# Optimization experiments

Hardware: AMD Instinct MI355X
Metric: run time of the kernel (lower is better)

The kernel has to match this reference:

```python
import jax, jax.numpy as jnp
import numpy as np

H = 12          # num heads
D = 768         # embed dim
HD = D // H     # head dim
SCALE = HD ** -0.5
NEG = -(3.0 ** 39)  # matches torch's triu(1) * -3.0**39 mask value


def setup_inputs() -> dict:
    key = jax.random.key(0)
    ks = jax.random.split(key, 9)
    B, S = 4, 1024
    lim = 1.0 / np.sqrt(D)
    def lin(k):
        kw, kb = jax.random.split(k)
        W = jax.random.uniform(kw, (D, D), jnp.float32, -lim, lim)  # [out,in]
        b = jax.random.uniform(kb, (D,), jnp.float32, -lim, lim)
        return W, b
    Wq, bq = lin(ks[0]); Wk, bk = lin(ks[1]); Wv, bv = lin(ks[2]); Wo, bo = lin(ks[3])
    hidden_states = jax.random.normal(ks[4], (B, S, D), jnp.float32)
    return {"hidden_states": hidden_states,
            "Wq": Wq, "bq": bq, "Wk": Wk, "bk": bk,
            "Wv": Wv, "bv": bv, "Wo": Wo, "bo": bo}


def reference(hidden_states, Wq, bq, Wk, bk, Wv, bv, Wo, bo):
    B, S, _ = hidden_states.shape
    split = lambda x: x.reshape(B, S, H, HD).transpose(0, 2, 1, 3)  # [B,H,S,HD]
    q = split(hidden_states @ Wq.T + bq) * SCALE
    k = split(hidden_states @ Wk.T + bk)
    v = split(hidden_states @ Wv.T + bv)
    scores = jnp.einsum('bhqd,bhkd->bhqk', q, k)
    causal_mask = jnp.triu(jnp.full((S, S), NEG, hidden_states.dtype), k=1)
    scores = scores + causal_mask  # broadcast over [B,H]
    probs = jax.nn.softmax(scores, axis=-1)
    out = jnp.einsum('bhqk,bhkd->bhqd', probs, v)
    out = out.transpose(0, 2, 1, 3).reshape(B, S, H * HD)
    return out @ Wo.T + bo
```

## Files before the change

kernel.cpp:

```cpp
#include <hip/hip_runtime.h>

#define NH 12
#define DM 768
#define HD 64
#define BB 4
#define SS 1024
#define MTOT (BB*SS)
#define ATT_SCALE 0.125f
#define NEGMASK (-4.0525551530189755e18f)

typedef __attribute__((ext_vector_type(8))) short short8;
typedef __attribute__((ext_vector_type(4))) float floatx4;
typedef __attribute__((ext_vector_type(4))) unsigned short ushort4v;

__device__ __forceinline__ float bf2f(unsigned short u){
    union { unsigned int i; float f; } x; x.i = ((unsigned int)u) << 16; return x.f;
}
__device__ __forceinline__ unsigned short f2bf(float f){
    union { float f; unsigned int i; } x; x.f = f;
    unsigned int i = x.i;
    return (unsigned short)((i + 0x7FFFu + ((i >> 16) & 1u)) >> 16);
}

#define XQ4 (MTOT*DM/4)
#define WQ4 (DM*DM/4)

__global__ __launch_bounds__(256) void convert_bf16(
    const float* __restrict__ X,
    const float* __restrict__ Wq, const float* __restrict__ Wk,
    const float* __restrict__ Wv, const float* __restrict__ Wo,
    unsigned short* __restrict__ Xb,
    unsigned short* __restrict__ Wqb, unsigned short* __restrict__ Wkb,
    unsigned short* __restrict__ Wvb, unsigned short* __restrict__ Wob)
{
    const int idx = blockIdx.x * 256 + threadIdx.x;
    const float* s; unsigned short* d; int off;
    if (idx < XQ4) { s = X; d = Xb; off = idx; }
    else {
        const int r = idx - XQ4;
        const int wsel = r / WQ4;
        off = r - wsel * WQ4;
        s = (wsel==0)?Wq:(wsel==1)?Wk:(wsel==2)?Wv:Wo;
        d = (wsel==0)?Wqb:(wsel==1)?Wkb:(wsel==2)?Wvb:Wob;
    }
    const float4 v = ((const float4*)s)[off];
    ushort4v o;
    o[0] = f2bf(v.x); o[1] = f2bf(v.y); o[2] = f2bf(v.z); o[3] = f2bf(v.w);
    ((ushort4v*)d)[off] = o;
}

__global__ __launch_bounds__(256) void qkv_mfma(
    const unsigned short* __restrict__ Xb,
    const unsigned short* __restrict__ Wqb,
    const unsigned short* __restrict__ Wkb,
    const unsigned short* __restrict__ Wvb,
    const float* __restrict__ bq, const float* __restrict__ bk,
    const float* __restrict__ bv,
    unsigned short* __restrict__ qout,
    unsigned short* __restrict__ kout,
    unsigned short* __restrict__ vout)
{
    const int which = blockIdx.z;
    const int n0 = blockIdx.x * 128;
    const int m0 = blockIdx.y * 128;
    const unsigned short* W = (which==0) ? Wqb : (which==1) ? Wkb : Wvb;
    const float* bias = (which==0) ? bq : (which==1) ? bk : bv;
    unsigned short* out = (which==0) ? qout : (which==1) ? kout : vout;
    const float scl = (which==0) ? ATT_SCALE : 1.0f;

    __shared__ unsigned short As[128*32];
    __shared__ unsigned short Bs[128*32];

    const int t = threadIdx.x;
    const int w = t >> 6, lane = t & 63;
    const int c = lane & 15, g = lane >> 4;
    const int wr = w >> 1, wc = w & 1;

    floatx4 acc[4][4] = {};

    const int srow = lane >> 2;
    const int ske  = (lane & 3) * 8;

    for (int k0 = 0; k0 < DM; k0 += 32) {
        __syncthreads();
        #pragma unroll
        for (int j = 0; j < 2; ++j) {
            const int row = w*32 + j*16 + srow;
            __builtin_amdgcn_global_load_lds(
                (const __attribute__((address_space(1))) unsigned int*)
                    (Xb + (size_t)(m0 + row) * DM + k0 + ske),
                (__attribute__((address_space(3))) unsigned int*)
                    (As + (w*32 + j*16) * 32),
                16, 0, 0);
            __builtin_amdgcn_global_load_lds(
                (const __attribute__((address_space(1))) unsigned int*)
                    (W + (size_t)(n0 + row) * DM + k0 + ske),
                (__attribute__((address_space(3))) unsigned int*)
                    (Bs + (w*32 + j*16) * 32),
                16, 0, 0);
        }
        __syncthreads();

        short8 af[4], bfr[4];
        #pragma unroll
        for (int mi = 0; mi < 4; ++mi)
            af[mi] = *(const short8*)(As + (wr*64 + mi*16 + c)*32 + g*8);
        #pragma unroll
        for (int ni = 0; ni < 4; ++ni)
            bfr[ni] = *(const short8*)(Bs + (wc*64 + ni*16 + c)*32 + g*8);
        #pragma unroll
        for (int mi = 0; mi < 4; ++mi)
            #pragma unroll
            for (int ni = 0; ni < 4; ++ni)
                acc[mi][ni] = __builtin_amdgcn_mfma_f32_16x16x32_bf16(
                    af[mi], bfr[ni], acc[mi][ni], 0, 0, 0);
    }

    #pragma unroll
    for (int mi = 0; mi < 4; ++mi) {
        #pragma unroll
        for (int r = 0; r < 4; ++r) {
            const int m = m0 + wr*64 + mi*16 + g*4 + r;
            const int b = m >> 10, s = m & 1023;
            #pragma unroll
            for (int ni = 0; ni < 4; ++ni) {
                const int n = n0 + wc*64 + ni*16 + c;
                const int h = n >> 6, hd = n & 63;
                const float val = (acc[mi][ni][r] + bias[n]) * scl;
                out[(((size_t)(b*NH + h))*SS + s)*HD + hd] = f2bf(val);
            }
        }
    }
}

__global__ __launch_bounds__(256) void attn_mfma(
    const unsigned short* __restrict__ Q,
    const unsigned short* __restrict__ K,
    const unsigned short* __restrict__ V,
    unsigned short* __restrict__ O)
{
    const int bh = blockIdx.x;
    const int qb = blockIdx.y * 64;
    const unsigned short* Qp = Q + (size_t)bh * SS * HD;
    const unsigned short* Kp = K + (size_t)bh * SS * HD;
    const unsigned short* Vp = V + (size_t)bh * SS * HD;

    __shared__ unsigned short Vt[64 * 72];
    __shared__ unsigned short Pl[4][16 * 72];

    const int t    = threadIdx.x;
    const int w    = t >> 6;
    const int lane = t & 63;
    const int c    = lane & 15;
    const int g    = lane >> 4;

    short8 qf[2];
    #pragma unroll
    for (int st = 0; st < 2; ++st)
        qf[st] = *(const short8*)(Qp + (size_t)(qb + w*16 + c) * HD + g*8 + 32*st);

    floatx4 Oacc[4] = {};
    float m_r[4], l_r[4];
    #pragma unroll
    for (int r = 0; r < 4; ++r) { m_r[r] = -INFINITY; l_r[r] = 0.0f; }

    const int ntile = qb / 64 + 1;
    for (int kt = 0; kt < ntile; ++kt) {
        const int k0 = kt * 64;

        __syncthreads();
        {
            const int kk = t >> 2;
            const int d0 = (t & 3) * 16;
            const unsigned short* vp = Vp + (size_t)(k0 + kk) * HD + d0;
            short8 v0 = *(const short8*)(vp);
            short8 v1 = *(const short8*)(vp + 8);
            #pragma unroll
            for (int j = 0; j < 8; ++j) {
                Vt[(d0 + j    ) * 72 + kk] = (unsigned short)v0[j];
                Vt[(d0 + j + 8) * 72 + kk] = (unsigned short)v1[j];
            }
        }
        __syncthreads();

        floatx4 Sacc[4] = {};
        #pragma unroll
        for (int nf = 0; nf < 4; ++nf) {
            #pragma unroll
            for (int st = 0; st < 2; ++st) {
                const short8 kf = *(const short8*)(Kp + (size_t)(k0 + nf*16 + c) * HD + g*8 + 32*st);
                Sacc[nf] = __builtin_amdgcn_mfma_f32_16x16x32_bf16(qf[st], kf, Sacc[nf], 0, 0, 0);
            }
        }

        if (k0 + 63 > qb + w*16) {
            #pragma unroll
            for (int nf = 0; nf < 4; ++nf) {
                const int col = k0 + nf*16 + c;
                #pragma unroll
                for (int r = 0; r < 4; ++r) {
                    const int row = qb + w*16 + g*4 + r;
                    if (col > row) Sacc[nf][r] += NEGMASK;
                }
            }
        }

        float alpha[4];
        #pragma unroll
        for (int r = 0; r < 4; ++r) {
            float mx = Sacc[0][r];
            mx = fmaxf(mx, Sacc[1][r]);
            mx = fmaxf(mx, Sacc[2][r]);
            mx = fmaxf(mx, Sacc[3][r]);
            #pragma unroll
            for (int msk = 1; msk < 16; msk <<= 1)
                mx = fmaxf(mx, __shfl_xor(mx, msk, 64));
            const float mnew = fmaxf(m_r[r], mx);
            alpha[r] = __expf(m_r[r] - mnew);
            float sum = 0.0f;
            #pragma unroll
            for (int nf = 0; nf < 4; ++nf) {
                const float p = __expf(Sacc[nf][r] - mnew);
                Sacc[nf][r] = p;
                sum += p;
            }
            #pragma unroll
            for (int msk = 1; msk < 16; msk <<= 1)
                sum += __shfl_xor(sum, msk, 64);
            l_r[r] = l_r[r] * alpha[r] + sum;
            m_r[r] = mnew;
            #pragma unroll
            for (int nf = 0; nf < 4; ++nf) Oacc[nf][r] *= alpha[r];
        }

        unsigned short* pw = Pl[w];
        #pragma unroll
        for (int r = 0; r < 4; ++r)
            #pragma unroll
            for (int nf = 0; nf < 4; ++nf)
                pw[(g*4 + r) * 72 + nf*16 + c] = f2bf(Sacc[nf][r]);

        #pragma unroll
        for (int st = 0; st < 2; ++st) {
            const short8 pf = *(const short8*)(pw + c * 72 + g*8 + 32*st);
            #pragma unroll
            for (int nf = 0; nf < 4; ++nf) {
                const short8 vf = *(const short8*)(Vt + (nf*16 + c) * 72 + g*8 + 32*st);
                Oacc[nf] = __builtin_amdgcn_mfma_f32_16x16x32_bf16(pf, vf, Oacc[nf], 0, 0, 0);
            }
        }
    }

    const int b = bh / NH, h = bh % NH;
    #pragma unroll
    for (int r = 0; r < 4; ++r) {
        const float inv = 1.0f / l_r[r];
        const int s = qb + w*16 + g*4 + r;
        #pragma unroll
        for (int nf = 0; nf < 4; ++nf)
            O[((size_t)(b*SS + s))*DM + h*HD + nf*16 + c] = f2bf(Oacc[nf][r] * inv);
    }
}

__global__ __launch_bounds__(256) void out_mfma(
    const unsigned short* __restrict__ A,
    const unsigned short* __restrict__ Wb,
    const float* __restrict__ bias,
    float* __restrict__ outf)
{
    const int n0 = blockIdx.x * 128;
    const int m0 = blockIdx.y * 128;

    __shared__ unsigned short As[128*32];
    __shared__ unsigned short Bs[128*32];

    const int t = threadIdx.x;
    const int w = t >> 6, lane = t & 63;
    const int c = lane & 15, g = lane >> 4;
    const int wr = w >> 1, wc = w & 1;

    floatx4 acc[4][4] = {};

    const int srow = lane >> 2;
    const int ske  = (lane & 3) * 8;

    for (int k0 = 0; k0 < DM; k0 += 32) {
        __syncthreads();
        #pragma unroll
        for (int j = 0; j < 2; ++j) {
            const int row = w*32 + j*16 + srow;
            __builtin_amdgcn_global_load_lds(
                (const __attribute__((address_space(1))) unsigned int*)
                    (A + (size_t)(m0 + row) * DM + k0 + ske),
                (__attribute__((address_space(3))) unsigned int*)
                    (As + (w*32 + j*16) * 32),
                16, 0, 0);
            __builtin_amdgcn_global_load_lds(
                (const __attribute__((address_space(1))) unsigned int*)
                    (Wb + (size_t)(n0 + row) * DM + k0 + ske),
                (__attribute__((address_space(3))) unsigned int*)
                    (Bs + (w*32 + j*16) * 32),
                16, 0, 0);
        }
        __syncthreads();

        short8 af[4], bfr[4];
        #pragma unroll
        for (int mi = 0; mi < 4; ++mi)
            af[mi] = *(const short8*)(As + (wr*64 + mi*16 + c)*32 + g*8);
        #pragma unroll
        for (int ni = 0; ni < 4; ++ni)
            bfr[ni] = *(const short8*)(Bs + (wc*64 + ni*16 + c)*32 + g*8);
        #pragma unroll
        for (int mi = 0; mi < 4; ++mi)
            #pragma unroll
            for (int ni = 0; ni < 4; ++ni)
                acc[mi][ni] = __builtin_amdgcn_mfma_f32_16x16x32_bf16(
                    af[mi], bfr[ni], acc[mi][ni], 0, 0, 0);
    }

    #pragma unroll
    for (int mi = 0; mi < 4; ++mi) {
        #pragma unroll
        for (int r = 0; r < 4; ++r) {
            const int m = m0 + wr*64 + mi*16 + g*4 + r;
            #pragma unroll
            for (int ni = 0; ni < 4; ++ni) {
                const int n = n0 + wc*64 + ni*16 + c;
                outf[(size_t)m * DM + n] = acc[mi][ni][r] + bias[n];
            }
        }
    }
}

extern "C" void kernel_launch(void* const* d_in, const int* in_sizes, int n_in,
                              void* d_out, int out_size, void* d_ws, size_t ws_size,
                              hipStream_t stream) {
    const float* X  = (const float*)d_in[0];
    const float* Wq = (const float*)d_in[1];
    const float* bq = (const float*)d_in[2];
    const float* Wk = (const float*)d_in[3];
    const float* bk = (const float*)d_in[4];
    const float* Wv = (const float*)d_in[5];
    const float* bv = (const float*)d_in[6];
    const float* Wo = (const float*)d_in[7];
    const float* bo = (const float*)d_in[8];
    float* out = (float*)d_out;

    const size_t elems = (size_t)MTOT * DM;
    const size_t welems = (size_t)DM * DM;
    unsigned short* q    = (unsigned short*)d_ws;
    unsigned short* k    = q    + elems;
    unsigned short* v    = k    + elems;
    unsigned short* attn = v    + elems;
    unsigned short* xb   = attn + elems;
    unsigned short* wqb  = xb   + elems;
    unsigned short* wkb  = wqb  + welems;
    unsigned short* wvb  = wkb  + welems;
    unsigned short* wob  = wvb  + welems;

    convert_bf16<<<dim3((XQ4 + 4*WQ4) / 256), 256, 0, stream>>>(
        X, Wq, Wk, Wv, Wo, xb, wqb, wkb, wvb, wob);
    qkv_mfma<<<dim3(6, 32, 3), 256, 0, stream>>>(
        xb, wqb, wkb, wvb, bq, bk, bv, q, k, v);
    attn_mfma<<<dim3(48, 16), 256, 0, stream>>>(q, k, v, attn);
    out_mfma<<<dim3(6, 32), 256, 0, stream>>>(attn, wob, bo, out);
}
```

Measured before the change: 181.3 us.

## Write V transposed from QKV GEMM, use single-wave attention blocks, shrink GEMM tiles

The QKV projection now writes V in a transposed [b,h,d,s] layout, so the attention kernel loads V fragments straight from global memory and no longer transposes through shared memory with barriers. Attention is recast as one 64-thread wave per 16-query tile, with the longest causal rows scheduled first, giving many more and better balanced blocks. Masking is applied only on the last key tile. Both GEMMs use 128x64 tiles instead of 128x128, doubling the grid for occupancy at the cost of less operand reuse. The transposed V store is strided and uncoalesced, and V fragments are re-read per query tile from global or cache with no LDS sharing.

```diff
diff --git a/kernel.cpp b/kernel.cpp
--- a/kernel.cpp
+++ b/kernel.cpp
@@ -61,22 +61,21 @@
     unsigned short* __restrict__ vout)
 {
     const int which = blockIdx.z;
-    const int n0 = blockIdx.x * 128;
+    const int n0 = blockIdx.x * 64;
     const int m0 = blockIdx.y * 128;
     const unsigned short* W = (which==0) ? Wqb : (which==1) ? Wkb : Wvb;
     const float* bias = (which==0) ? bq : (which==1) ? bk : bv;
-    unsigned short* out = (which==0) ? qout : (which==1) ? kout : vout;
     const float scl = (which==0) ? ATT_SCALE : 1.0f;
 
     __shared__ unsigned short As[128*32];
-    __shared__ unsigned short Bs[128*32];
+    __shared__ unsigned short Bs[64*32];
 
     const int t = threadIdx.x;
     const int w = t >> 6, lane = t & 63;
     const int c = lane & 15, g = lane >> 4;
     const int wr = w >> 1, wc = w & 1;
 
-    floatx4 acc[4][4] = {};
+    floatx4 acc[4][2] = {};
 
     const int srow = lane >> 2;
     const int ske  = (lane & 3) * 8;
@@ -92,26 +91,29 @@
                 (__attribute__((address_space(3))) unsigned int*)
                     (As + (w*32 + j*16) * 32),
                 16, 0, 0);
+        }
+        {
+            const int row = w*16 + srow;
             __builtin_amdgcn_global_load_lds(
                 (const __attribute__((address_space(1))) unsigned int*)
                     (W + (size_t)(n0 + row) * DM + k0 + ske),
                 (__attribute__((address_space(3))) unsigned int*)
-                    (Bs + (w*32 + j*16) * 32),
+                    (Bs + (w*16) * 32),
                 16, 0, 0);
         }
         __syncthreads();
 
-        short8 af[4], bfr[4];
+        short8 af[4], bfr[2];
         #pragma unroll
         for (int mi = 0; mi < 4; ++mi)
             af[mi] = *(const short8*)(As + (wr*64 + mi*16 + c)*32 + g*8);
         #pragma unroll
-        for (int ni = 0; ni < 4; ++ni)
-            bfr[ni] = *(const short8*)(Bs + (wc*64 + ni*16 + c)*32 + g*8);
+        for (int ni = 0; ni < 2; ++ni)
+            bfr[ni] = *(const short8*)(Bs + (wc*32 + ni*16 + c)*32 + g*8);
         #pragma unroll
         for (int mi = 0; mi < 4; ++mi)
             #pragma unroll
-            for (int ni = 0; ni < 4; ++ni)
+            for (int ni = 0; ni < 2; ++ni)
                 acc[mi][ni] = __builtin_amdgcn_mfma_f32_16x16x32_bf16(
                     af[mi], bfr[ni], acc[mi][ni], 0, 0, 0);
     }
@@ -123,100 +125,96 @@
             const int m = m0 + wr*64 + mi*16 + g*4 + r;
             const int b = m >> 10, s = m & 1023;
             #pragma unroll
-            for (int ni = 0; ni < 4; ++ni) {
-                const int n = n0 + wc*64 + ni*16 + c;
+            for (int ni = 0; ni < 2; ++ni) {
+                const int n = n0 + wc*32 + ni*16 + c;
                 const int h = n >> 6, hd = n & 63;
                 const float val = (acc[mi][ni][r] + bias[n]) * scl;
-                out[(((size_t)(b*NH + h))*SS + s)*HD + hd] = f2bf(val);
+                if (which == 2)
+                    vout[(((size_t)(b*NH + h))*HD + hd)*SS + s] = f2bf(val);
+                else if (which == 1)
+                    kout[(((size_t)(b*NH + h))*SS + s)*HD + hd] = f2bf(val);
+                else
+                    qout[(((size_t)(b*NH + h))*SS + s)*HD + hd] = f2bf(val);
             }
         }
     }
 }
 
-__global__ __launch_bounds__(256) void attn_mfma(
+__global__ __launch_bounds__(64) void attn_mfma(
     const unsigned short* __restrict__ Q,
     const unsigned short* __restrict__ K,
-    const unsigned short* __restrict__ V,
+    const unsigned short* __restrict__ VT,
     unsigned short* __restrict__ O)
 {
-    const int bh = blockIdx.x;
-    const int qb = blockIdx.y * 64;
-    const unsigned short* Qp = Q + (size_t)bh * SS * HD;
-    const unsigned short* Kp = K + (size_t)bh * SS * HD;
-    const unsigned short* Vp = V + (size_t)bh * SS * HD;
-
-    __shared__ unsigned short Vt[64 * 72];
-    __shared__ unsigned short Pl[4][16 * 72];
-
-    const int t    = threadIdx.x;
-    const int w    = t >> 6;
-    const int lane = t & 63;
+    const int idx = blockIdx.x;
+    const int bh  = idx % 48;
+    const int z   = 63 - (idx / 48);
+    const int q0  = z * 16;
+
+    const unsigned short* Qp  = Q  + (size_t)bh * SS * HD;
+    const unsigned short* Kp  = K  + (size_t)bh * SS * HD;
+    const unsigned short* VTp = VT + (size_t)bh * HD * SS;
+
+    __shared__ unsigned short Pl[16 * 72];
+
+    const int lane = threadIdx.x;
     const int c    = lane & 15;
     const int g    = lane >> 4;
 
     short8 qf[2];
     #pragma unroll
     for (int st = 0; st < 2; ++st)
-        qf[st] = *(const short8*)(Qp + (size_t)(qb + w*16 + c) * HD + g*8 + 32*st);
+        qf[st] = *(const short8*)(Qp + (size_t)(q0 + c) * HD + g*8 + 32*st);
 
     floatx4 Oacc[4] = {};
     float m_r[4], l_r[4];
     #pragma unroll
     for (int r = 0; r < 4; ++r) { m_r[r] = -INFINITY; l_r[r] = 0.0f; }
 
-    const int ntile = qb / 64 + 1;
+    const int ntile = z/4 + 1;
     for (int kt = 0; kt < ntile; ++kt) {
         const int k0 = kt * 64;
 
-        __syncthreads();
-        {
-            const int kk = t >> 2;
-            const int d0 = (t & 3) * 16;
-            const unsigned short* vp = Vp + (size_t)(k0 + kk) * HD + d0;
-            short8 v0 = *(const short8*)(vp);
-            short8 v1 = *(const short8*)(vp + 8);
-            #pragma unroll
-            for (int j = 0; j < 8; ++j) {
-                Vt[(d0 + j    ) * 72 + kk] = (unsigned short)v0[j];
-                Vt[(d0 + j + 8) * 72 + kk] = (unsigned short)v1[j];
-            }
-        }
-        __syncthreads();
+        short8 kf[4][2], vf[2][4];
+        #pragma unroll
+        for (int nf = 0; nf < 4; ++nf)
+            #pragma unroll
+            for (int st = 0; st < 2; ++st)
+                kf[nf][st] = *(const short8*)(Kp + (size_t)(k0 + nf*16 + c) * HD + g*8 + 32*st);
+        #pragma unroll
+        for (int st = 0; st < 2; ++st)
+            #pragma unroll
+            for (int nf = 0; nf < 4; ++nf)
+                vf[st][nf] = *(const short8*)(VTp + (size_t)(nf*16 + c) * SS + k0 + g*8 + 32*st);
 
         floatx4 Sacc[4] = {};
         #pragma unroll
-        for (int nf = 0; nf < 4; ++nf) {
-            #pragma unroll
-            for (int st = 0; st < 2; ++st) {
-                const short8 kf = *(const short8*)(Kp + (size_t)(k0 + nf*16 + c) * HD + g*8 + 32*st);
-                Sacc[nf] = __builtin_amdgcn_mfma_f32_16x16x32_bf16(qf[st], kf, Sacc[nf], 0, 0, 0);
-            }
-        }
-
-        if (k0 + 63 > qb + w*16) {
+        for (int nf = 0; nf < 4; ++nf)
+            #pragma unroll
+            for (int st = 0; st < 2; ++st)
+                Sacc[nf] = __builtin_amdgcn_mfma_f32_16x16x32_bf16(qf[st], kf[nf][st], Sacc[nf], 0, 0, 0);
+
+        if (kt == ntile - 1) {
             #pragma unroll
             for (int nf = 0; nf < 4; ++nf) {
                 const int col = k0 + nf*16 + c;
                 #pragma unroll
                 for (int r = 0; r < 4; ++r) {
-                    const int row = qb + w*16 + g*4 + r;
+                    const int row = q0 + g*4 + r;
                     if (col > row) Sacc[nf][r] += NEGMASK;
                 }
             }
         }
 
-        float alpha[4];
         #pragma unroll
         for (int r = 0; r < 4; ++r) {
-            float mx = Sacc[0][r];
-            mx = fmaxf(mx, Sacc[1][r]);
-            mx = fmaxf(mx, Sacc[2][r]);
-            mx = fmaxf(mx, Sacc[3][r]);
+            float mx = fmaxf(fmaxf(Sacc[0][r], Sacc[1][r]),
+                             fmaxf(Sacc[2][r], Sacc[3][r]));
             #pragma unroll
             for (int msk = 1; msk < 16; msk <<= 1)
                 mx = fmaxf(mx, __shfl_xor(mx, msk, 64));
             const float mnew = fmaxf(m_r[r], mx);
-            alpha[r] = __expf(m_r[r] - mnew);
+            const float alpha = __expf(m_r[r] - mnew);
             float sum = 0.0f;
             #pragma unroll
             for (int nf = 0; nf < 4; ++nf) {
@@ -227,27 +225,24 @@
             #pragma unroll
             for (int msk = 1; msk < 16; msk <<= 1)
                 sum += __shfl_xor(sum, msk, 64);
-            l_r[r] = l_r[r] * alpha[r] + sum;
+            l_r[r] = l_r[r] * alpha + sum;
             m_r[r] = mnew;
             #pragma unroll
-            for (int nf = 0; nf < 4; ++nf) Oacc[nf][r] *= alpha[r];
-        }
-
-        unsigned short* pw = Pl[w];
+            for (int nf = 0; nf < 4; ++nf) Oacc[nf][r] *= alpha;
+        }
+
         #pragma unroll
         for (int r = 0; r < 4; ++r)
             #pragma unroll
             for (int nf = 0; nf < 4; ++nf)
-                pw[(g*4 + r) * 72 + nf*16 + c] = f2bf(Sacc[nf][r]);
+                Pl[(g*4 + r) * 72 + nf*16 + c] = f2bf(Sacc[nf][r]);
 
         #pragma unroll
         for (int st = 0; st < 2; ++st) {
-            const short8 pf = *(const short8*)(pw + c * 72 + g*8 + 32*st);
-            #pragma unroll
-            for (int nf = 0; nf < 4; ++nf) {
-                const short8 vf = *(const short8*)(Vt + (nf*16 + c) * 72 + g*8 + 32*st);
-                Oacc[nf] = __builtin_amdgcn_mfma_f32_16x16x32_bf16(pf, vf, Oacc[nf], 0, 0, 0);
-            }
+            const short8 pf = *(const short8*)(Pl + c * 72 + g*8 + 32*st);
+            #pragma unroll
+            for (int nf = 0; nf < 4; ++nf)
+                Oacc[nf] = __builtin_amdgcn_mfma_f32_16x16x32_bf16(pf, vf[st][nf], Oacc[nf], 0, 0, 0);
         }
     }
 
@@ -255,7 +250,7 @@
     #pragma unroll
     for (int r = 0; r < 4; ++r) {
         const float inv = 1.0f / l_r[r];
-        const int s = qb + w*16 + g*4 + r;
+        const int s = q0 + g*4 + r;
         #pragma unroll
         for (int nf = 0; nf < 4; ++nf)
             O[((size_t)(b*SS + s))*DM + h*HD + nf*16 + c] = f2bf(Oacc[nf][r] * inv);
@@ -268,18 +263,18 @@
     const float* __restrict__ bias,
     float* __restrict__ outf)
 {
-    const int n0 = blockIdx.x * 128;
+    const int n0 = blockIdx.x * 64;
     const int m0 = blockIdx.y * 128;
 
     __shared__ unsigned short As[128*32];
-    __shared__ unsigned short Bs[128*32];
+    __shared__ unsigned short Bs[64*32];
 
     const int t = threadIdx.x;
     const int w = t >> 6, lane = t & 63;
     const int c = lane & 15, g = lane >> 4;
     const int wr = w >> 1, wc = w & 1;
 
-    floatx4 acc[4][4] = {};
+    floatx4 acc[4][2] = {};
 
     const int srow = lane >> 2;
     const int ske  = (lane & 3) * 8;
@@ -295,26 +290,29 @@
                 (__attribute__((address_space(3))) unsigned int*)
                     (As + (w*32 + j*16) * 32),
                 16, 0, 0);
+        }
+        {
+            const int row = w*16 + srow;
             __builtin_amdgcn_global_load_lds(
                 (const __attribute__((address_space(1))) unsigned int*)
                     (Wb + (size_t)(n0 + row) * DM + k0 + ske),
                 (__attribute__((address_space(3))) unsigned int*)
-                    (Bs + (w*32 + j*16) * 32),
+                    (Bs + (w*16) * 32),
                 16, 0, 0);
         }
         __syncthreads();
 
-        short8 af[4], bfr[4];
+        short8 af[4], bfr[2];
         #pragma unroll
         for (int mi = 0; mi < 4; ++mi)
             af[mi] = *(const short8*)(As + (wr*64 + mi*16 + c)*32 + g*8);
         #pragma unroll
-        for (int ni = 0; ni < 4; ++ni)
-            bfr[ni] = *(const short8*)(Bs + (wc*64 + ni*16 + c)*32 + g*8);
+        for (int ni = 0; ni < 2; ++ni)
+            bfr[ni] = *(const short8*)(Bs + (wc*32 + ni*16 + c)*32 + g*8);
         #pragma unroll
         for (int mi = 0; mi < 4; ++mi)
             #pragma unroll
-            for (int ni = 0; ni < 4; ++ni)
+            for (int ni = 0; ni < 2; ++ni)
                 acc[mi][ni] = __builtin_amdgcn_mfma_f32_16x16x32_bf16(
                     af[mi], bfr[ni], acc[mi][ni], 0, 0, 0);
     }
@@ -325,8 +323,8 @@
         for (int r = 0; r < 4; ++r) {
             const int m = m0 + wr*64 + mi*16 + g*4 + r;
             #pragma unroll
-            for (int ni = 0; ni < 4; ++ni) {
-                const int n = n0 + wc*64 + ni*16 + c;
+            for (int ni = 0; ni < 2; ++ni) {
+                const int n = n0 + wc*32 + ni*16 + c;
                 outf[(size_t)m * DM + n] = acc[mi][ni][r] + bias[n];
             }
         }
@@ -351,8 +349,8 @@
     const size_t welems = (size_t)DM * DM;
     unsigned short* q    = (unsigned short*)d_ws;
     unsigned short* k    = q    + elems;
-    unsigned short* v    = k    + elems;
-    unsigned short* attn = v    + elems;
+    unsigned short* vt   = k    + elems;
+    unsigned short* attn = vt   + elems;
     unsigned short* xb   = attn + elems;
     unsigned short* wqb  = xb   + elems;
     unsigned short* wkb  = wqb  + welems;
@@ -361,8 +359,8 @@
 
     convert_bf16<<<dim3((XQ4 + 4*WQ4) / 256), 256, 0, stream>>>(
         X, Wq, Wk, Wv, Wo, xb, wqb, wkb, wvb, wob);
-    qkv_mfma<<<dim3(6, 32, 3), 256, 0, stream>>>(
-        xb, wqb, wkb, wvb, bq, bk, bv, q, k, v);
-    attn_mfma<<<dim3(48, 16), 256, 0, stream>>>(q, k, v, attn);
-    out_mfma<<<dim3(6, 32), 256, 0, stream>>>(attn, wob, bo, out);
-}
+    qkv_mfma<<<dim3(12, 32, 3), 256, 0, stream>>>(
+        xb, wqb, wkb, wvb, bq, bk, bv, q, k, vt);
+    attn_mfma<<<dim3(3072), 64, 0, stream>>>(q, k, vt, attn);
+    out_mfma<<<dim3(12, 32), 256, 0, stream>>>(attn, wob, bo, out);
+}
```

Measured after the change: 189.9 us. 1.05x slower.
